# Kernel optimization log

Measured on AMD Instinct MI355X. Metric: run time of the kernel, lower is better.

## Reference

```python
import jax, jax.numpy as jnp
import numpy as np

B, T = 128, 64          # batch, episode length
OB, AC, L, H = 32, 8, 128, 256  # ob_dim, ac_dim, latent_dim, mlp hidden
N_SUB = 4               # fixed Dopri5 substeps per interval (replaces adaptive PID controller)


def setup_inputs() -> dict:
    key = jax.random.key(0)
    ks = jax.random.split(key, 12)
    g = lambda k, shape, fan: jax.random.normal(k, shape, jnp.float32) / np.sqrt(fan)
    return {
        "ob": jax.random.normal(ks[0], (B, OB), jnp.float32),
        "acs": jax.random.normal(ks[1], (B, T, AC), jnp.float32),
        # strictly increasing timestamps (cumsum of uniform increments)
        "times": jnp.cumsum(jax.random.uniform(ks[2], (B, T), jnp.float32, 0.02, 0.1), axis=1),
        # ob encoder MLP (OB -> H -> L), relu hidden, identity out
        "We0": g(ks[3], (H, OB), OB), "be0": jnp.zeros((H,), jnp.float32),
        "We1": g(ks[4], (L, H), H), "be1": jnp.zeros((L,), jnp.float32),
        # latent dynamics MLP (L -> H -> H -> L)
        "Wd0": g(ks[5], (H, L), L), "bd0": jnp.zeros((H,), jnp.float32),
        "Wd1": g(ks[6], (H, H), H), "bd1": jnp.zeros((H,), jnp.float32),
        "Wd2": g(ks[7], (L, H), H), "bd2": jnp.zeros((L,), jnp.float32),
        # ob decoder MLP (L -> H -> OB)
        "Wo0": g(ks[8], (H, L), L), "bo0": jnp.zeros((H,), jnp.float32),
        "Wo1": g(ks[9], (OB, H), H), "bo1": jnp.zeros((OB,), jnp.float32),
        # GRU cell (input=AC, hidden=L), equinox layout: gates [r, z, n]
        "Wih": g(ks[10], (3 * L, AC), AC), "Whh": g(ks[11], (3 * L, L), L),
        "bih": jnp.zeros((3 * L,), jnp.float32), "bn": jnp.zeros((L,), jnp.float32),
    }


def reference(ob, acs, times, We0, be0, We1, be1, Wd0, bd0, Wd1, bd1, Wd2, bd2,
              Wo0, bo0, Wo1, bo1, Wih, Whh, bih, bn):
    def f(y):  # dynamics MLP on batched latent (B, L) -> (B, L)
        h1 = jax.nn.relu(y @ Wd0.T + bd0)
        h2 = jax.nn.relu(h1 @ Wd1.T + bd1)
        return h2 @ Wd2.T + bd2

    def gru(x, h):  # equinox GRUCell math, batched
        ir, iz, inn = jnp.split(x @ Wih.T + bih, 3, axis=-1)
        hr, hz, hn = jnp.split(h @ Whh.T, 3, axis=-1)
        r = jax.nn.sigmoid(ir + hr)
        z = jax.nn.sigmoid(iz + hz)
        n = jnp.tanh(inn + r * (hn + bn))
        return (1.0 - z) * n + z * h

    def dopri5_step(y, h):  # one Dopri5 (RK45) step, h: (B, 1) per-sample step size
        k1 = f(y)
        k2 = f(y + h * (0.2 * k1))
        k3 = f(y + h * (3/40 * k1 + 9/40 * k2))
        k4 = f(y + h * (44/45 * k1 - 56/15 * k2 + 32/9 * k3))
        k5 = f(y + h * (19372/6561 * k1 - 25360/2187 * k2 + 64448/6561 * k3 - 212/729 * k4))
        k6 = f(y + h * (9017/3168 * k1 - 355/33 * k2 + 46732/5247 * k3 + 49/176 * k4 - 5103/18656 * k5))
        return y + h * (35/384 * k1 + 500/1113 * k3 + 125/192 * k4 - 2187/6784 * k5 + 11/84 * k6)

    def integrate(y, dt):  # integrate latent ODE from 0 to dt with N_SUB fixed Dopri5 steps
        h = (dt / N_SUB)[:, None]
        return jax.lax.fori_loop(0, N_SUB, lambda i, yy: dopri5_step(yy, h), y)

    # encode first observation, consume first action
    latent0 = jax.nn.relu(ob @ We0.T + be0) @ We1.T + be1  # (B, L)
    latent0 = gru(acs[:, 0], latent0)

    dts = jnp.diff(times, axis=1)  # (B, T-1)

    def step(latent, xs):
        ac, dt = xs
        latent = integrate(latent, dt)
        latent = gru(ac, latent)
        return latent, latent

    xs = (jnp.swapaxes(acs[:, 1:], 0, 1), dts.T)  # time-major for scan
    _, lat_seq = jax.lax.scan(step, latent0, xs)  # (T-1, B, L)

    latents = jnp.concatenate([latent0[None], lat_seq], axis=0)  # (T, B, L)
    latents = jnp.swapaxes(latents, 0, 1)  # (B, T, L)

    h1 = jax.nn.relu(latents @ Wo0.T + bo0)
    return h1 @ Wo1.T + bo1  # (B, T, OB)
```

## Files before the change

### kernel.cpp

```cpp
#include <hip/hip_runtime.h>
#include <stdint.h>

#define NBATCH 128
#define NT     64
#define OBD    32
#define ACD    8
#define LDIM   128
#define HDIM   256

typedef _Float16 h2 __attribute__((ext_vector_type(2)));
typedef float    f4 __attribute__((ext_vector_type(4)));

#if defined(__has_builtin)
#  if __has_builtin(__builtin_amdgcn_fdot2)
#    define HAVE_FDOT2 1
#  endif
#endif

__device__ __forceinline__ float dot2f(h2 a, h2 b, float c) {
#ifdef HAVE_FDOT2
  return __builtin_amdgcn_fdot2(a, b, c, false);
#else
  return c + (float)a[0] * (float)b[0] + (float)a[1] * (float)b[1];
#endif
}

__device__ __forceinline__ h2 pkh(float a, float b) {
  h2 r; r[0] = (_Float16)a; r[1] = (_Float16)b; return r;
}

__device__ __forceinline__ h2 bch(float x) { return __builtin_bit_cast(h2, x); }

__device__ __forceinline__ float sigmf(float x) { return 1.0f / (1.0f + expf(-x)); }

#define DOT4(W, I, Q) \
    a0 = dot2f(W[4*(I)+0], bch(Q.x), a0); \
    a1 = dot2f(W[4*(I)+1], bch(Q.y), a1); \
    a2 = dot2f(W[4*(I)+2], bch(Q.z), a2); \
    a3 = dot2f(W[4*(I)+3], bch(Q.w), a3);

__global__ __launch_bounds__(512, 2)
void ode_rnn_kernel(const float* __restrict__ ob,   const float* __restrict__ acs,
                    const float* __restrict__ times,
                    const float* __restrict__ We0,  const float* __restrict__ be0,
                    const float* __restrict__ We1,  const float* __restrict__ be1,
                    const float* __restrict__ Wd0,  const float* __restrict__ bd0,
                    const float* __restrict__ Wd1,  const float* __restrict__ bd1,
                    const float* __restrict__ Wd2,  const float* __restrict__ bd2,
                    const float* __restrict__ Wo0,  const float* __restrict__ bo0,
                    const float* __restrict__ Wo1,  const float* __restrict__ bo1,
                    const float* __restrict__ Wih,  const float* __restrict__ Whh,
                    const float* __restrict__ bih,  const float* __restrict__ bn,
                    float* __restrict__ out)
{
  const int t    = threadIdx.x;
  const int b    = blockIdx.x;
  const int p    = t >> 1;
  const int sub  = t & 1;
  const int r3   = t >> 2;
  const int ksub = t & 3;

  __shared__ __align__(16) float s_lat[LDIM];
  __shared__ __align__(16) float s_k[6][LDIM];
  __shared__ __align__(16) float s_gz[LDIM];
  __shared__ __align__(16) float s_gin[LDIM];
  __shared__ __align__(16) float s_ghn[LDIM];
  __shared__ __align__(16) float s_tmp[HDIM];
  __shared__ __align__(16) float s_obs[OBD];
  __shared__ __align__(16) float s_times[NT];
  __shared__ __align__(16) float s_acs[NT * ACD];
  __shared__ __align__(16) h2    s_in16[LDIM / 2];
  __shared__ __align__(16) h2    s_a16[HDIM / 2];
  __shared__ __align__(16) h2    s_b16[HDIM / 2];

  h2 w0[32], w1[64], w2[32], q0[32], q1[8];
  {
    const float2* pp = (const float2*)(Wd0 + p * LDIM + sub * 64);
#pragma unroll
    for (int i = 0; i < 32; ++i) { float2 v = pp[i]; w0[i] = pkh(v.x, v.y); }
  }
  {
    const float2* pp = (const float2*)(Wd1 + p * HDIM + sub * 128);
#pragma unroll
    for (int i = 0; i < 64; ++i) { float2 v = pp[i]; w1[i] = pkh(v.x, v.y); }
  }
  {
    const float2* pp = (const float2*)(Wd2 + r3 * HDIM + ksub * 64);
#pragma unroll
    for (int i = 0; i < 32; ++i) { float2 v = pp[i]; w2[i] = pkh(v.x, v.y); }
  }
  {
    const float2* pp = (const float2*)(Wo0 + p * LDIM + sub * 64);
#pragma unroll
    for (int i = 0; i < 32; ++i) { float2 v = pp[i]; q0[i] = pkh(v.x, v.y); }
  }
  {
    const float2* pp = (const float2*)(Wo1 + (t >> 4) * HDIM + (t & 15) * 16);
#pragma unroll
    for (int i = 0; i < 8; ++i) { float2 v = pp[i]; q1[i] = pkh(v.x, v.y); }
  }
  float wi[8];
  if (t < 3 * LDIM) {
#pragma unroll
    for (int j = 0; j < ACD; ++j) wi[j] = Wih[t * ACD + j];
  } else {
#pragma unroll
    for (int j = 0; j < ACD; ++j) wi[j] = 0.0f;
  }

  const float bb0 = bd0[p];
  const float bb1 = bd1[p];
  const float bb2 = bd2[r3];
  const float rb0 = bo0[p];
  const float rb1 = bo1[t >> 4];
  const float gbA = (t < 3 * LDIM) ? bih[t] : 0.0f;
  const float bnr = (t < LDIM) ? bn[t] : 0.0f;

  auto feval = [&](int s) {
    float a0, a1, a2, a3, v;
    a0 = a1 = a2 = a3 = 0.0f;
    {
      const f4* src = ((const f4*)s_in16) + sub * 8;
#pragma unroll
      for (int i = 0; i < 8; ++i) { f4 q = src[i]; DOT4(w0, i, q) }
    }
    v = a0 + a1 + a2 + a3;
    v += __shfl_xor(v, 1);
    v = fmaxf(v + bb0, 0.0f);
    {
      float ov = __shfl_xor(v, 2);
      if ((t & 3) == 0) s_a16[t >> 2] = pkh(v, ov);
    }
    __syncthreads();
    a0 = a1 = a2 = a3 = 0.0f;
    {
      const f4* src = ((const f4*)s_a16) + sub * 16;
#pragma unroll
      for (int i = 0; i < 16; ++i) { f4 q = src[i]; DOT4(w1, i, q) }
    }
    v = a0 + a1 + a2 + a3;
    v += __shfl_xor(v, 1);
    v = fmaxf(v + bb1, 0.0f);
    {
      float ov = __shfl_xor(v, 2);
      if ((t & 3) == 0) s_b16[t >> 2] = pkh(v, ov);
    }
    __syncthreads();
    a0 = a1 = a2 = a3 = 0.0f;
    {
      const f4* src = ((const f4*)s_b16) + ksub * 8;
#pragma unroll
      for (int i = 0; i < 8; ++i) { f4 q = src[i]; DOT4(w2, i, q) }
    }
    v = a0 + a1 + a2 + a3;
    v += __shfl_xor(v, 1);
    v += __shfl_xor(v, 2);
    if ((t & 3) == 0) s_k[s][r3] = v + bb2;
    __syncthreads();
  };

  auto substep = [&](float hs) {
#pragma unroll 1
    for (int s = 0; s < 6; ++s) {
      if (s && t < LDIM) {
        float z = s_lat[t];
        if      (s == 1) z += hs * (0.2f * s_k[0][t]);
        else if (s == 2) z += hs * ((3.0f/40.0f)*s_k[0][t] + (9.0f/40.0f)*s_k[1][t]);
        else if (s == 3) z += hs * ((44.0f/45.0f)*s_k[0][t] - (56.0f/15.0f)*s_k[1][t]
                                  + (32.0f/9.0f)*s_k[2][t]);
        else if (s == 4) z += hs * ((19372.0f/6561.0f)*s_k[0][t] - (25360.0f/2187.0f)*s_k[1][t]
                                  + (64448.0f/6561.0f)*s_k[2][t] - (212.0f/729.0f)*s_k[3][t]);
        else             z += hs * ((9017.0f/3168.0f)*s_k[0][t] - (355.0f/33.0f)*s_k[1][t]
                                  + (46732.0f/5247.0f)*s_k[2][t] + (49.0f/176.0f)*s_k[3][t]
                                  - (5103.0f/18656.0f)*s_k[4][t]);
        float ov = __shfl_xor(z, 1);
        if (!(t & 1)) s_in16[t >> 1] = pkh(z, ov);
      }
      __syncthreads();
      feval(s);
    }
    if (t < LDIM) {
      float y = s_lat[t];
      y += hs * ((35.0f/384.0f)*s_k[0][t] + (500.0f/1113.0f)*s_k[2][t]
               + (125.0f/192.0f)*s_k[3][t] - (2187.0f/6784.0f)*s_k[4][t]
               + (11.0f/84.0f)*s_k[5][t]);
      s_lat[t] = y;
      float ov = __shfl_xor(y, 1);
      if (!(t & 1)) s_in16[t >> 1] = pkh(y, ov);
    }
  };

  auto gru = [&](int ts) {
    __syncthreads();
    float ig = gbA, hg = 0.0f;
    if (t < 3 * LDIM) {
      const float* xa = s_acs + ts * ACD;
#pragma unroll
      for (int j = 0; j < ACD; ++j) ig += wi[j] * xa[j];
      const f4* wh = (const f4*)(Whh + t * LDIM);
      const f4* xl = (const f4*)s_lat;
#pragma unroll
      for (int k2 = 0; k2 < LDIM / 4; ++k2) {
        f4 w = wh[k2], x = xl[k2];
        hg += w.x*x.x + w.y*x.y + w.z*x.z + w.w*x.w;
      }
    }
    if (t >= LDIM && t < 2 * LDIM)          s_gz[t - LDIM] = ig + hg;
    else if (t >= 2 * LDIM && t < 3 * LDIM) { s_gin[t - 2*LDIM] = ig; s_ghn[t - 2*LDIM] = hg; }
    __syncthreads();
    if (t < LDIM) {
      float rg = sigmf(ig + hg);
      float zg = sigmf(s_gz[t]);
      float ng = tanhf(s_gin[t] + rg * (s_ghn[t] + bnr));
      float y  = (1.0f - zg) * ng + zg * s_lat[t];
      s_lat[t] = y;
      float ov = __shfl_xor(y, 1);
      if (!(t & 1)) s_in16[t >> 1] = pkh(y, ov);
    }
  };

  auto decode = [&](int ts) {
    __syncthreads();
    float a0 = 0, a1 = 0, a2 = 0, a3 = 0, v;
    {
      const f4* src = ((const f4*)s_in16) + sub * 8;
#pragma unroll
      for (int i = 0; i < 8; ++i) { f4 q = src[i]; DOT4(q0, i, q) }
    }
    v = a0 + a1 + a2 + a3;
    v += __shfl_xor(v, 1);
    v = fmaxf(v + rb0, 0.0f);
    {
      float ov = __shfl_xor(v, 2);
      if ((t & 3) == 0) s_a16[t >> 2] = pkh(v, ov);
    }
    __syncthreads();
    a0 = a1 = a2 = a3 = 0;
    {
      const f4* src = ((const f4*)s_a16) + (t & 15) * 2;
#pragma unroll
      for (int i = 0; i < 2; ++i) {
        f4 q = src[i];
        a0 = dot2f(q1[4*i+0], bch(q.x), a0);
        a1 = dot2f(q1[4*i+1], bch(q.y), a1);
        a2 = dot2f(q1[4*i+2], bch(q.z), a2);
        a3 = dot2f(q1[4*i+3], bch(q.w), a3);
      }
    }
    v = a0 + a1 + a2 + a3;
    v += __shfl_xor(v, 1);
    v += __shfl_xor(v, 2);
    v += __shfl_xor(v, 4);
    v += __shfl_xor(v, 8);
    if ((t & 15) == 0) out[((size_t)b * NT + ts) * OBD + (t >> 4)] = v + rb1;
  };

  if (t < OBD) s_obs[t] = ob[b * OBD + t];
  if (t < NT)  s_times[t] = times[b * NT + t];
  s_acs[t] = acs[(size_t)b * NT * ACD + t];
  __syncthreads();
  if (t < HDIM) {
    float acc = be0[t];
    const float* wr = We0 + t * OBD;
#pragma unroll
    for (int j = 0; j < OBD; ++j) acc += wr[j] * s_obs[j];
    s_tmp[t] = fmaxf(acc, 0.0f);
  }
  __syncthreads();
  {
    const f4* wr = (const f4*)(We1 + r3 * HDIM + ksub * 64);
    const f4* xs = (const f4*)(s_tmp + ksub * 64);
    float acc = 0.0f;
#pragma unroll
    for (int k = 0; k < 16; ++k) {
      f4 w = wr[k], x = xs[k];
      acc += w.x*x.x + w.y*x.y + w.z*x.z + w.w*x.w;
    }
    acc += __shfl_xor(acc, 1);
    acc += __shfl_xor(acc, 2);
    if ((t & 3) == 0) s_lat[r3] = acc + be1[r3];
  }

  gru(0);
  decode(0);

#pragma unroll 1
  for (int ts = 1; ts < NT; ++ts) {
    float hs = 0.25f * (s_times[ts] - s_times[ts - 1]);
#pragma unroll 1
    for (int su = 0; su < 4; ++su) substep(hs);
    gru(ts);
    decode(ts);
  }
}

extern "C" void kernel_launch(void* const* d_in, const int* in_sizes, int n_in,
                              void* d_out, int out_size, void* d_ws, size_t ws_size,
                              hipStream_t stream) {
  (void)in_sizes; (void)n_in; (void)d_ws; (void)ws_size; (void)out_size;
  const float* ob    = (const float*)d_in[0];
  const float* acs   = (const float*)d_in[1];
  const float* times = (const float*)d_in[2];
  const float* We0   = (const float*)d_in[3];
  const float* be0   = (const float*)d_in[4];
  const float* We1   = (const float*)d_in[5];
  const float* be1   = (const float*)d_in[6];
  const float* Wd0   = (const float*)d_in[7];
  const float* bd0   = (const float*)d_in[8];
  const float* Wd1   = (const float*)d_in[9];
  const float* bd1   = (const float*)d_in[10];
  const float* Wd2   = (const float*)d_in[11];
  const float* bd2   = (const float*)d_in[12];
  const float* Wo0   = (const float*)d_in[13];
  const float* bo0   = (const float*)d_in[14];
  const float* Wo1   = (const float*)d_in[15];
  const float* bo1   = (const float*)d_in[16];
  const float* Wih   = (const float*)d_in[17];
  const float* Whh   = (const float*)d_in[18];
  const float* bih   = (const float*)d_in[19];
  const float* bn    = (const float*)d_in[20];

  ode_rnn_kernel<<<dim3(NBATCH), dim3(512), 0, stream>>>(
      ob, acs, times, We0, be0, We1, be1, Wd0, bd0, Wd1, bd1, Wd2, bd2,
      Wo0, bo0, Wo1, bo1, Wih, Whh, bih, bn, (float*)d_out);
}
```

Before: 2.605 ms.

## Fuse Runge-Kutta stage combination into the dynamics output layer and pad shared buffer

```diff
diff --git a/kernel.cpp b/kernel.cpp
--- a/kernel.cpp
+++ b/kernel.cpp
@@ -39,7 +39,7 @@
     a2 = dot2f(W[4*(I)+2], bch(Q.z), a2); \
     a3 = dot2f(W[4*(I)+3], bch(Q.w), a3);
 
-__global__ __launch_bounds__(512, 2)
+__global__ __launch_bounds__(512, 1)
 void ode_rnn_kernel(const float* __restrict__ ob,   const float* __restrict__ acs,
                     const float* __restrict__ times,
                     const float* __restrict__ We0,  const float* __restrict__ be0,
@@ -61,7 +61,7 @@
   const int ksub = t & 3;
 
   __shared__ __align__(16) float s_lat[LDIM];
-  __shared__ __align__(16) float s_k[6][LDIM];
+  __shared__ __align__(16) float s_k[5][LDIM];
   __shared__ __align__(16) float s_gz[LDIM];
   __shared__ __align__(16) float s_gin[LDIM];
   __shared__ __align__(16) float s_ghn[LDIM];
@@ -71,7 +71,7 @@
   __shared__ __align__(16) float s_acs[NT * ACD];
   __shared__ __align__(16) h2    s_in16[LDIM / 2];
   __shared__ __align__(16) h2    s_a16[HDIM / 2];
-  __shared__ __align__(16) h2    s_b16[HDIM / 2];
+  __shared__ __align__(16) h2    s_b16[HDIM / 2 + 24];
 
   h2 w0[32], w1[64], w2[32], q0[32], q1[8];
   {
@@ -116,77 +116,67 @@
   const float gbA = (t < 3 * LDIM) ? bih[t] : 0.0f;
   const float bnr = (t < LDIM) ? bn[t] : 0.0f;
 
-  auto feval = [&](int s) {
-    float a0, a1, a2, a3, v;
-    a0 = a1 = a2 = a3 = 0.0f;
-    {
-      const f4* src = ((const f4*)s_in16) + sub * 8;
-#pragma unroll
-      for (int i = 0; i < 8; ++i) { f4 q = src[i]; DOT4(w0, i, q) }
-    }
-    v = a0 + a1 + a2 + a3;
-    v += __shfl_xor(v, 1);
-    v = fmaxf(v + bb0, 0.0f);
-    {
-      float ov = __shfl_xor(v, 2);
-      if ((t & 3) == 0) s_a16[t >> 2] = pkh(v, ov);
-    }
-    __syncthreads();
-    a0 = a1 = a2 = a3 = 0.0f;
-    {
-      const f4* src = ((const f4*)s_a16) + sub * 16;
-#pragma unroll
-      for (int i = 0; i < 16; ++i) { f4 q = src[i]; DOT4(w1, i, q) }
-    }
-    v = a0 + a1 + a2 + a3;
-    v += __shfl_xor(v, 1);
-    v = fmaxf(v + bb1, 0.0f);
-    {
-      float ov = __shfl_xor(v, 2);
-      if ((t & 3) == 0) s_b16[t >> 2] = pkh(v, ov);
-    }
-    __syncthreads();
-    a0 = a1 = a2 = a3 = 0.0f;
-    {
-      const f4* src = ((const f4*)s_b16) + ksub * 8;
-#pragma unroll
-      for (int i = 0; i < 8; ++i) { f4 q = src[i]; DOT4(w2, i, q) }
-    }
-    v = a0 + a1 + a2 + a3;
-    v += __shfl_xor(v, 1);
-    v += __shfl_xor(v, 2);
-    if ((t & 3) == 0) s_k[s][r3] = v + bb2;
-    __syncthreads();
-  };
-
   auto substep = [&](float hs) {
-#pragma unroll 1
+#pragma unroll
     for (int s = 0; s < 6; ++s) {
-      if (s && t < LDIM) {
-        float z = s_lat[t];
-        if      (s == 1) z += hs * (0.2f * s_k[0][t]);
-        else if (s == 2) z += hs * ((3.0f/40.0f)*s_k[0][t] + (9.0f/40.0f)*s_k[1][t]);
-        else if (s == 3) z += hs * ((44.0f/45.0f)*s_k[0][t] - (56.0f/15.0f)*s_k[1][t]
-                                  + (32.0f/9.0f)*s_k[2][t]);
-        else if (s == 4) z += hs * ((19372.0f/6561.0f)*s_k[0][t] - (25360.0f/2187.0f)*s_k[1][t]
-                                  + (64448.0f/6561.0f)*s_k[2][t] - (212.0f/729.0f)*s_k[3][t]);
-        else             z += hs * ((9017.0f/3168.0f)*s_k[0][t] - (355.0f/33.0f)*s_k[1][t]
-                                  + (46732.0f/5247.0f)*s_k[2][t] + (49.0f/176.0f)*s_k[3][t]
-                                  - (5103.0f/18656.0f)*s_k[4][t]);
-        float ov = __shfl_xor(z, 1);
-        if (!(t & 1)) s_in16[t >> 1] = pkh(z, ov);
-      }
+      float a0, a1, a2, a3, v;
+      a0 = a1 = a2 = a3 = 0.0f;
+      {
+        const f4* src = ((const f4*)s_in16) + sub * 8;
+#pragma unroll
+        for (int i = 0; i < 8; ++i) { f4 q = src[i]; DOT4(w0, i, q) }
+      }
+      v = a0 + a1 + a2 + a3;
+      v += __shfl_xor(v, 1);
+      v = fmaxf(v + bb0, 0.0f);
+      { float ov = __shfl_xor(v, 2); if ((t & 3) == 0) s_a16[t >> 2] = pkh(v, ov); }
       __syncthreads();
-      feval(s);
-    }
-    if (t < LDIM) {
-      float y = s_lat[t];
-      y += hs * ((35.0f/384.0f)*s_k[0][t] + (500.0f/1113.0f)*s_k[2][t]
-               + (125.0f/192.0f)*s_k[3][t] - (2187.0f/6784.0f)*s_k[4][t]
-               + (11.0f/84.0f)*s_k[5][t]);
-      s_lat[t] = y;
-      float ov = __shfl_xor(y, 1);
-      if (!(t & 1)) s_in16[t >> 1] = pkh(y, ov);
+      a0 = a1 = a2 = a3 = 0.0f;
+      {
+        const f4* src = ((const f4*)s_a16) + sub * 16;
+#pragma unroll
+        for (int i = 0; i < 16; ++i) { f4 q = src[i]; DOT4(w1, i, q) }
+      }
+      v = a0 + a1 + a2 + a3;
+      v += __shfl_xor(v, 1);
+      v = fmaxf(v + bb1, 0.0f);
+      { float ov = __shfl_xor(v, 2);
+        if ((t & 3) == 0) s_b16[(t >> 2) + ((t >> 7) << 3)] = pkh(v, ov); }
+      __syncthreads();
+      a0 = a1 = a2 = a3 = 0.0f;
+      {
+        const f4* src = ((const f4*)s_b16) + ksub * 10;
+#pragma unroll
+        for (int i = 0; i < 8; ++i) { f4 q = src[i]; DOT4(w2, i, q) }
+      }
+      v = a0 + a1 + a2 + a3;
+      v += __shfl_xor(v, 1);
+      v += __shfl_xor(v, 2);
+      float kv = v + bb2;
+      if (s < 5 && (t & 3) == 0) s_k[s][r3] = kv;
+      float base = s_lat[r3];
+      float z;
+      if (s == 0)
+        z = base + hs * (0.2f * kv);
+      else if (s == 1)
+        z = base + hs * ((3.0f/40.0f)*s_k[0][r3] + (9.0f/40.0f)*kv);
+      else if (s == 2)
+        z = base + hs * ((44.0f/45.0f)*s_k[0][r3] - (56.0f/15.0f)*s_k[1][r3]
+                       + (32.0f/9.0f)*kv);
+      else if (s == 3)
+        z = base + hs * ((19372.0f/6561.0f)*s_k[0][r3] - (25360.0f/2187.0f)*s_k[1][r3]
+                       + (64448.0f/6561.0f)*s_k[2][r3] - (212.0f/729.0f)*kv);
+      else if (s == 4)
+        z = base + hs * ((9017.0f/3168.0f)*s_k[0][r3] - (355.0f/33.0f)*s_k[1][r3]
+                       + (46732.0f/5247.0f)*s_k[2][r3] + (49.0f/176.0f)*s_k[3][r3]
+                       - (5103.0f/18656.0f)*kv);
+      else
+        z = base + hs * ((35.0f/384.0f)*s_k[0][r3] + (500.0f/1113.0f)*s_k[2][r3]
+                       + (125.0f/192.0f)*s_k[3][r3] - (2187.0f/6784.0f)*s_k[4][r3]
+                       + (11.0f/84.0f)*kv);
+      { float ov = __shfl_xor(z, 4); if ((t & 7) == 0) s_in16[t >> 3] = pkh(z, ov); }
+      if (s == 5 && (t & 3) == 0) s_lat[r3] = z;
+      __syncthreads();
     }
   };
 
@@ -230,10 +220,7 @@
     v = a0 + a1 + a2 + a3;
     v += __shfl_xor(v, 1);
     v = fmaxf(v + rb0, 0.0f);
-    {
-      float ov = __shfl_xor(v, 2);
-      if ((t & 3) == 0) s_a16[t >> 2] = pkh(v, ov);
-    }
+    { float ov = __shfl_xor(v, 2); if ((t & 3) == 0) s_a16[t >> 2] = pkh(v, ov); }
     __syncthreads();
     a0 = a1 = a2 = a3 = 0;
     {
@@ -253,6 +240,7 @@
     v += __shfl_xor(v, 4);
     v += __shfl_xor(v, 8);
     if ((t & 15) == 0) out[((size_t)b * NT + ts) * OBD + (t >> 4)] = v + rb1;
+    __syncthreads();
   };
 
   if (t < OBD) s_obs[t] = ob[b * OBD + t];
```

Result: faster. 2.461 ms (-5.5%).
